# Kernel tuning notes

Hardware: AMD Instinct MI355X
Metric: run time of the kernel (lower is better)

Reference implementation:

```python
import jax, jax.numpy as jnp
import numpy as np

D_MODEL, N_HEADS, LATENT, ROPE = 4096, 128, 512, 64
HEAD_DIM = D_MODEL // N_HEADS  # 32
B, S = 2, 1024


def setup_inputs() -> dict:
    key = jax.random.key(0)
    ks = jax.random.split(key, 9)
    def w(k, i, o):
        return jax.random.normal(k, (i, o), dtype=jnp.float32) * (1.0 / np.sqrt(i))
    return {
        "x": jax.random.normal(ks[0], (B, S, D_MODEL), dtype=jnp.float32),
        "Wq_down": w(ks[1], D_MODEL, LATENT),
        "Wq_up": w(ks[2], LATENT, N_HEADS * HEAD_DIM),
        "Wq_rope": w(ks[3], D_MODEL, N_HEADS * ROPE),
        "Wkv_down": w(ks[4], D_MODEL, LATENT),
        "Wk_up": w(ks[5], LATENT, N_HEADS * HEAD_DIM),
        "Wv_up": w(ks[6], LATENT, N_HEADS * HEAD_DIM),
        "Wk_rope": w(ks[7], D_MODEL, ROPE),
        "Wo": w(ks[8], N_HEADS * HEAD_DIM, D_MODEL),
    }


def reference(x, Wq_down, Wq_up, Wq_rope, Wkv_down, Wk_up, Wv_up, Wk_rope, Wo):
    b, s, _ = x.shape
    # latent down-projections
    c_q = x @ Wq_down                                   # [B,S,latent]
    c_kv = x @ Wkv_down                                 # [B,S,latent]
    # up-projections, reshaped to per-head
    q_c = (c_q @ Wq_up).reshape(b, s, N_HEADS, HEAD_DIM)    # [B,S,H,Dh]
    q_r = (x @ Wq_rope).reshape(b, s, N_HEADS, ROPE)        # [B,S,H,Dr]
    k_c = (c_kv @ Wk_up).reshape(b, s, N_HEADS, HEAD_DIM)   # [B,S,H,Dh]
    v_c = (c_kv @ Wv_up).reshape(b, s, N_HEADS, HEAD_DIM)   # [B,S,H,Dh]
    k_r = x @ Wk_rope                                       # [B,S,Dr] shared over heads
    scale = jnp.asarray((HEAD_DIM + ROPE) ** 0.5, x.dtype)
    # scores = q.k with q=[q_c|q_r], k=[k_c|k_r(broadcast)] -> split the dot product
    scores = (jnp.einsum("bqhd,bkhd->bhqk", q_c, k_c)
              + jnp.einsum("bqhd,bkd->bhqk", q_r, k_r)) / scale  # [B,H,S,S]
    attn = jax.nn.softmax(scores, axis=-1)
    out = jnp.einsum("bhqk,bkhd->bqhd", attn, v_c)          # [B,S,H,Dh]
    out = out.reshape(b, s, N_HEADS * HEAD_DIM)
    return out @ Wo                                         # [B,S,d_model]
```

## Files before the change

kernel.cpp:

```cpp
#include <hip/hip_runtime.h>
#include <hip/hip_bf16.h>
#include <math.h>

#define D_MODEL 4096
#define N_HEADS 128
#define LATENT  512
#define ROPE_D  64
#define HEAD_D  32
#define BATCH   2
#define SEQ     1024
#define NTOK    (BATCH*SEQ)

typedef unsigned short u16;
typedef __attribute__((ext_vector_type(8))) short bf16x8;
typedef __attribute__((ext_vector_type(4))) float f32x4;

__device__ __forceinline__ u16 f2bf(float f) {
    union { float f; unsigned u; } v; v.f = f;
    unsigned r = (v.u + 0x7fffu + ((v.u >> 16) & 1u)) >> 16;
    return (u16)r;
}

__device__ __forceinline__ void gl_lds16(const u16* g, u16* l) {
    __builtin_amdgcn_global_load_lds(
        (const __attribute__((address_space(1))) unsigned int*)g,
        (__attribute__((address_space(3))) unsigned int*)l, 16, 0, 0);
}

__device__ __forceinline__ void castT_tile(const float* __restrict__ W,
                                           u16* __restrict__ Wt,
                                           int K, int N, int jx, int jy,
                                           float (*tile)[33])
{
    const int tid = threadIdx.x;
    const int j0 = jx * 32, i0 = jy * 32;
    {
        int r = tid >> 3, c4 = (tid & 7) << 2;
        float4 v = *(const float4*)(W + (size_t)(i0 + r) * N + j0 + c4);
        tile[r][c4 + 0] = v.x; tile[r][c4 + 1] = v.y;
        tile[r][c4 + 2] = v.z; tile[r][c4 + 3] = v.w;
    }
    __syncthreads();
    {
        int n = tid >> 3, k4 = (tid & 7) << 2;
        u16 o[4] = { f2bf(tile[k4 + 0][n]), f2bf(tile[k4 + 1][n]),
                     f2bf(tile[k4 + 2][n]), f2bf(tile[k4 + 3][n]) };
        *(uint2*)(Wt + (size_t)(j0 + n) * K + i0 + k4) = *(uint2*)o;
    }
}

template<int MODE>
__device__ __forceinline__ void gemm_core(const u16* __restrict__ A,
                                          const u16* __restrict__ Bt,
                                          void* __restrict__ Cout,
                                          int N, int K, int lda, int ldb, int ldc,
                                          int bm, int bn, u16* As, u16* Bs)
{
    const int tid  = threadIdx.x;
    const int lane = tid & 63;
    const int wave = tid >> 6;
    const int wr = wave >> 1, wc = wave & 1;
    const int l15 = lane & 15, lg = lane >> 4;

    f32x4 acc[4][4];
    #pragma unroll
    for (int i = 0; i < 4; ++i)
        #pragma unroll
        for (int j = 0; j < 4; ++j) acc[i][j] = (f32x4){0.f, 0.f, 0.f, 0.f};

    for (int kt = 0; kt < K; kt += 64) {
        __syncthreads();
        #pragma unroll
        for (int i = 0; i < 4; ++i) {
            int f = i * 256 + tid;
            int row = f >> 3, c = f & 7;
            int sc = c ^ (row & 7);
            gl_lds16(A + (size_t)(bm + row) * lda + kt + sc * 8, As + f * 8);
        }
        #pragma unroll
        for (int i = 0; i < 4; ++i) {
            int f = i * 256 + tid;
            int row = f >> 3, c = f & 7;
            int sc = c ^ (row & 7);
            gl_lds16(Bt + (size_t)(bn + row) * ldb + kt + sc * 8, Bs + f * 8);
        }
        __syncthreads();

        #pragma unroll
        for (int t = 0; t < 2; ++t) {
            bf16x8 af[4], bf[4];
            #pragma unroll
            for (int fm = 0; fm < 4; ++fm) {
                int row = wr * 64 + fm * 16 + l15;
                int c = (t * 4 + lg) ^ (row & 7);
                af[fm] = *(const bf16x8*)(As + row * 64 + c * 8);
            }
            #pragma unroll
            for (int fn = 0; fn < 4; ++fn) {
                int row = wc * 64 + fn * 16 + l15;
                int c = (t * 4 + lg) ^ (row & 7);
                bf[fn] = *(const bf16x8*)(Bs + row * 64 + c * 8);
            }
            #pragma unroll
            for (int fm = 0; fm < 4; ++fm)
                #pragma unroll
                for (int fn = 0; fn < 4; ++fn)
                    acc[fm][fn] = __builtin_amdgcn_mfma_f32_16x16x32_bf16(
                        af[fm], bf[fn], acc[fm][fn], 0, 0, 0);
        }
    }

    #pragma unroll
    for (int fm = 0; fm < 4; ++fm)
        #pragma unroll
        for (int fn = 0; fn < 4; ++fn)
            #pragma unroll
            for (int ri = 0; ri < 4; ++ri) {
                int row = bm + wr * 64 + fm * 16 + 4 * lg + ri;
                int col = bn + wc * 64 + fn * 16 + l15;
                if (col < N) {
                    float v = acc[fm][fn][ri];
                    if (MODE == 1) ((float*)Cout)[(size_t)row * ldc + col] = v;
                    else           ((u16*)Cout)[(size_t)row * ldc + col] = f2bf(v);
                }
            }
}

template<int MODE>
__global__ __launch_bounds__(256)
void gemm_bf16(const u16* __restrict__ A, const u16* __restrict__ Bt,
               void* __restrict__ Cout, int N, int K,
               int lda, int ldb, int ldc)
{
    __shared__ __align__(16) u16 As[128 * 64];
    __shared__ __align__(16) u16 Bs[128 * 64];
    const int nwg  = gridDim.x * gridDim.y;
    const int orig = blockIdx.y * gridDim.x + blockIdx.x;
    const int swz  = (orig & 7) * (nwg >> 3) + (orig >> 3);
    const int bm = (swz % gridDim.y) * 128;
    const int bn = (swz / gridDim.y) * 128;
    gemm_core<MODE>(A, Bt, Cout, N, K, lda, ldb, ldc, bm, bn, As, Bs);
}

__global__ __launch_bounds__(256)
void prep_kernel(const float* __restrict__ x, u16* __restrict__ xb,
                 const float* __restrict__ Wq_rope, const float* __restrict__ Wq_down,
                 const float* __restrict__ Wkv_down, const float* __restrict__ Wk_rope,
                 const float* __restrict__ Wk_up, const float* __restrict__ Wv_up,
                 const float* __restrict__ Wq_up,
                 u16* __restrict__ BigT, u16* __restrict__ UpT, u16* __restrict__ WuqT)
{
    __shared__ float tile[32][33];
    const int tid = threadIdx.x;
    int id = blockIdx.x;
    if (id < 4096) {
        size_t i = ((size_t)id * 256 + tid) * 8;
        float4 a = *(const float4*)(x + i);
        float4 b = *(const float4*)(x + i + 4);
        u16 o[8] = {f2bf(a.x), f2bf(a.y), f2bf(a.z), f2bf(a.w),
                    f2bf(b.x), f2bf(b.y), f2bf(b.z), f2bf(b.w)};
        *(bf16x8*)(xb + i) = *(bf16x8*)o;
        return;
    }
    id -= 4096;
    if (id < 32768) { castT_tile(Wq_rope, BigT, 4096, 8192, id & 255, id >> 8, tile); return; }
    id -= 32768;
    if (id < 2048) { castT_tile(Wq_down, BigT + (size_t)8192 * 4096, 4096, 512, id & 15, id >> 4, tile); return; }
    id -= 2048;
    if (id < 2048) { castT_tile(Wkv_down, BigT + (size_t)8704 * 4096, 4096, 512, id & 15, id >> 4, tile); return; }
    id -= 2048;
    if (id < 256) { castT_tile(Wk_rope, BigT + (size_t)9216 * 4096, 4096, 64, id & 1, id >> 1, tile); return; }
    id -= 256;
    if (id < 2048) { castT_tile(Wk_up, UpT, 512, 4096, id & 127, id >> 7, tile); return; }
    id -= 2048;
    if (id < 2048) { castT_tile(Wv_up, UpT + (size_t)4096 * 512, 512, 4096, id & 127, id >> 7, tile); return; }
    id -= 2048;
    if (id < 2048) { castT_tile(Wq_up, WuqT, 512, 4096, id & 127, id >> 7, tile); return; }
    id -= 2048;
    {
        u16* dst = BigT + ((size_t)9280 + id) * 4096;
        bf16x8 z = (bf16x8){0, 0, 0, 0, 0, 0, 0, 0};
        *(bf16x8*)(dst + tid * 8) = z;
        *(bf16x8*)(dst + 2048 + tid * 8) = z;
    }
}

__global__ __launch_bounds__(256)
void fused2_kernel(const u16* __restrict__ Cbig, const u16* __restrict__ UpT,
                   u16* __restrict__ C2, const u16* __restrict__ WuqT,
                   u16* __restrict__ q_c, const float* __restrict__ Wo,
                   u16* __restrict__ WoT)
{
    __shared__ __align__(16) u16 As[128 * 64];
    __shared__ __align__(16) u16 Bs[128 * 64];
    int id = blockIdx.x;
    if (id < 1024) {
        const int swz = (id & 7) * 128 + (id >> 3);
        const int bm = (swz & 15) * 128, bn = (swz >> 4) * 128;
        gemm_core<0>(Cbig + 8704, UpT, C2, 8192, 512, 9344, 512, 8192, bm, bn, As, Bs);
        return;
    }
    id -= 1024;
    if (id < 512) {
        const int swz = (id & 7) * 64 + (id >> 3);
        const int bm = (swz & 15) * 128, bn = (swz >> 4) * 128;
        gemm_core<0>(Cbig + 8192, WuqT, q_c, 4096, 512, 9344, 512, 4096, bm, bn, As, Bs);
        return;
    }
    id -= 512;
    {
        float (*tile)[33] = reinterpret_cast<float(*)[33]>(As);
        castT_tile(Wo, WoT, 4096, 4096, id & 127, id >> 7, tile);
    }
}

__global__ __launch_bounds__(256)
void vtrans_kernel(const u16* __restrict__ vc, u16* __restrict__ vt)
{
    __shared__ __align__(16) u16 tile[64][72];
    const int tid = threadIdx.x;
    const int c0 = blockIdx.x * 64;
    const int s0 = blockIdx.y * 64;
    const int b  = blockIdx.z;
    #pragma unroll
    for (int it = 0; it < 2; ++it) {
        int e = it * 256 + tid;
        int r = e >> 3, c8 = e & 7;
        *(bf16x8*)&tile[r][c8 * 8] =
            *(const bf16x8*)(vc + (size_t)(b * SEQ + s0 + r) * 8192 + c0 + c8 * 8);
    }
    __syncthreads();
    #pragma unroll
    for (int it = 0; it < 2; ++it) {
        int e = it * 256 + tid;
        int d = e >> 3, c8 = e & 7;
        u16 o[8];
        #pragma unroll
        for (int j = 0; j < 8; ++j) o[j] = tile[c8 * 8 + j][d];
        *(bf16x8*)(vt + (size_t)(b * D_MODEL + c0 + d) * SEQ + s0 + c8 * 8) = *(bf16x8*)o;
    }
}

__global__ __launch_bounds__(256)
void attn_kernel(const u16* __restrict__ q_c, const u16* __restrict__ q_r,
                 const u16* __restrict__ k_c, const u16* __restrict__ k_r,
                 const u16* __restrict__ vt,  u16* __restrict__ attn_out)
{
    __shared__ __align__(16) u16 s_kc[2][64 * 32];
    __shared__ __align__(16) u16 s_kr[2][64 * 64];
    __shared__ __align__(16) u16 s_vt[2][32 * 64];
    __shared__ __align__(16) u16 s_p[4][16 * 64];
    __shared__ __align__(16) u16 s_one[16 * 64];

    const int tid  = threadIdx.x;
    const int lane = tid & 63;
    const int w    = tid >> 6;
    const int l15  = lane & 15, lg = lane >> 4;
    const int q0 = blockIdx.x * 64;
    const int h  = blockIdx.y;
    const int b  = blockIdx.z;
    const size_t bS = (size_t)b * SEQ;
    const int hc = h * HEAD_D;
    const float c2 = 0.1020620726159658f * 1.44269504088896f;

    const int qrow = q0 + w * 16 + l15;
    const bf16x8 qf0 = *(const bf16x8*)(q_c + (bS + qrow) * 4096 + hc + lg * 8);
    const bf16x8 qf1 = *(const bf16x8*)(q_r + (bS + qrow) * 9344 + h * ROPE_D + lg * 8);
    const bf16x8 qf2 = *(const bf16x8*)(q_r + (bS + qrow) * 9344 + h * ROPE_D + 32 + lg * 8);

    float m2 = -1e30f;
    f32x4 oacc[3];
    oacc[0] = (f32x4){0.f, 0.f, 0.f, 0.f};
    oacc[1] = (f32x4){0.f, 0.f, 0.f, 0.f};
    oacc[2] = (f32x4){0.f, 0.f, 0.f, 0.f};

    auto stage = [&](int buf, int k0) {
        { int f = tid, r = f >> 2, c = f & 3;
          gl_lds16(k_c + (bS + k0 + r) * 8192 + hc + ((c ^ ((r >> 1) & 3)) << 3),
                   &s_kc[buf][f * 8]); }
        #pragma unroll
        for (int it = 0; it < 2; ++it) {
          int f = it * 256 + tid, r = f >> 3, c = f & 7;
          gl_lds16(k_r + (bS + k0 + r) * 9344 + ((c ^ (r & 7)) << 3),
                   &s_kr[buf][f * 8]); }
        { int f = tid, d = f >> 3, c = f & 7;
          gl_lds16(vt + ((size_t)b * D_MODEL + hc + d) * SEQ + k0 + ((c ^ (d & 7)) << 3),
                   &s_vt[buf][f * 8]); }
    };

    {
        unsigned v = (tid < 16) ? 0x3F803F80u : 0u;
        *(uint2*)&s_one[tid * 4] = make_uint2(v, v);
    }
    stage(0, 0);
    asm volatile("s_waitcnt vmcnt(0) lgkmcnt(0)" ::: "memory");
    __builtin_amdgcn_sched_barrier(0);
    __builtin_amdgcn_s_barrier();
    __builtin_amdgcn_sched_barrier(0);

    int cur = 0;
    for (int t = 0; t < SEQ / 64; ++t) {
        if (t + 1 < SEQ / 64) {
            stage(cur ^ 1, (t + 1) * 64);
            asm volatile("s_waitcnt vmcnt(4)" ::: "memory");
        } else {
            asm volatile("s_waitcnt vmcnt(0)" ::: "memory");
        }
        __builtin_amdgcn_sched_barrier(0);
        __builtin_amdgcn_s_barrier();
        __builtin_amdgcn_sched_barrier(0);

        f32x4 sc[4];
        #pragma unroll
        for (int fc = 0; fc < 4; ++fc) sc[fc] = (f32x4){0.f, 0.f, 0.f, 0.f};
        __builtin_amdgcn_s_setprio(1);
        #pragma unroll
        for (int fc = 0; fc < 4; ++fc) {
            int row = fc * 16 + l15;
            bf16x8 kb = *(const bf16x8*)&s_kc[cur][row * 32 + ((lg ^ ((row >> 1) & 3)) << 3)];
            sc[fc] = __builtin_amdgcn_mfma_f32_16x16x32_bf16(kb, qf0, sc[fc], 0, 0, 0);
        }
        #pragma unroll
        for (int tt = 0; tt < 2; ++tt) {
            bf16x8 qf = tt ? qf2 : qf1;
            #pragma unroll
            for (int fc = 0; fc < 4; ++fc) {
                int row = fc * 16 + l15;
                bf16x8 kb = *(const bf16x8*)&s_kr[cur][row * 64 + (((tt * 4 + lg) ^ (row & 7)) << 3)];
                sc[fc] = __builtin_amdgcn_mfma_f32_16x16x32_bf16(kb, qf, sc[fc], 0, 0, 0);
            }
        }
        __builtin_amdgcn_s_setprio(0);

        float a0 = fmaxf(fmaxf(sc[0][0], sc[0][1]), sc[0][2]);
        float a1 = fmaxf(fmaxf(sc[0][3], sc[1][0]), sc[1][1]);
        float a2 = fmaxf(fmaxf(sc[1][2], sc[1][3]), sc[2][0]);
        float a3 = fmaxf(fmaxf(sc[2][1], sc[2][2]), sc[2][3]);
        float a4 = fmaxf(fmaxf(sc[3][0], sc[3][1]), sc[3][2]);
        float b0 = fmaxf(fmaxf(a0, a1), a2);
        float b1 = fmaxf(fmaxf(a3, a4), sc[3][3]);
        float tmx = fmaxf(b0, b1);
        tmx = fmaxf(tmx, __shfl_xor(tmx, 16));
        tmx = fmaxf(tmx, __shfl_xor(tmx, 32));
        float tl2 = tmx * c2;
        if (!__all(tl2 <= m2 + 8.f)) {
            float mn = fmaxf(m2, tl2);
            float corr = exp2f(m2 - mn);
            m2 = mn;
            #pragma unroll
            for (int ri = 0; ri < 4; ++ri) {
                float cr = __shfl(corr, 4 * lg + ri);
                oacc[0][ri] *= cr; oacc[1][ri] *= cr; oacc[2][ri] *= cr;
            }
        }
        unsigned pk0[4], pk1[4];
        #pragma unroll
        for (int fc = 0; fc < 4; ++fc) {
            float p0 = exp2f(fmaf(sc[fc][0], c2, -m2));
            float p1 = exp2f(fmaf(sc[fc][1], c2, -m2));
            float p2 = exp2f(fmaf(sc[fc][2], c2, -m2));
            float p3 = exp2f(fmaf(sc[fc][3], c2, -m2));
            asm("v_cvt_pk_bf16_f32 %0, %1, %2" : "=v"(pk0[fc]) : "v"(p0), "v"(p1));
            asm("v_cvt_pk_bf16_f32 %0, %1, %2" : "=v"(pk1[fc]) : "v"(p2), "v"(p3));
        }
        #pragma unroll
        for (int fc = 0; fc < 4; ++fc) {
            int ch = (2 * fc + (lg >> 1)) ^ (l15 & 7);
            *(uint2*)&s_p[w][l15 * 64 + ch * 8 + 4 * (lg & 1)] =
                make_uint2(pk0[fc], pk1[fc]);
        }

        __builtin_amdgcn_s_setprio(1);
        #pragma unroll
        for (int t2 = 0; t2 < 2; ++t2) {
            bf16x8 pa = *(const bf16x8*)&s_p[w][l15 * 64 + (((t2 * 4 + lg) ^ (l15 & 7)) << 3)];
            #pragma unroll
            for (int fd = 0; fd < 2; ++fd) {
                int row = fd * 16 + l15;
                bf16x8 vb = *(const bf16x8*)&s_vt[cur][row * 64 + (((t2 * 4 + lg) ^ (row & 7)) << 3)];
                oacc[fd] = __builtin_amdgcn_mfma_f32_16x16x32_bf16(pa, vb, oacc[fd], 0, 0, 0);
            }
            bf16x8 vb1 = *(const bf16x8*)&s_one[l15 * 64 + (((t2 * 4 + lg) ^ (l15 & 7)) << 3)];
            oacc[2] = __builtin_amdgcn_mfma_f32_16x16x32_bf16(pa, vb1, oacc[2], 0, 0, 0);
        }
        __builtin_amdgcn_s_setprio(0);

        asm volatile("s_waitcnt lgkmcnt(0)" ::: "memory");
        __builtin_amdgcn_sched_barrier(0);
        __builtin_amdgcn_s_barrier();
        __builtin_amdgcn_sched_barrier(0);
        cur ^= 1;
    }

    #pragma unroll
    for (int ri = 0; ri < 4; ++ri) {
        float ls = __shfl(oacc[2][ri], lg << 4);
        float inv = 1.f / ls;
        int row = q0 + w * 16 + 4 * lg + ri;
        attn_out[(bS + row) * 4096 + hc + l15]      = f2bf(oacc[0][ri] * inv);
        attn_out[(bS + row) * 4096 + hc + 16 + l15] = f2bf(oacc[1][ri] * inv);
    }
}

extern "C" void kernel_launch(void* const* d_in, const int* in_sizes, int n_in,
                              void* d_out, int out_size, void* d_ws, size_t ws_size,
                              hipStream_t stream)
{
    (void)in_sizes; (void)n_in; (void)out_size; (void)ws_size;

    const float* x        = (const float*)d_in[0];
    const float* Wq_down  = (const float*)d_in[1];
    const float* Wq_up    = (const float*)d_in[2];
    const float* Wq_rope  = (const float*)d_in[3];
    const float* Wkv_down = (const float*)d_in[4];
    const float* Wk_up    = (const float*)d_in[5];
    const float* Wv_up    = (const float*)d_in[6];
    const float* Wk_rope  = (const float*)d_in[7];
    const float* Wo       = (const float*)d_in[8];

    u16* ws   = (u16*)d_ws;
    u16* xb   = ws;
    u16* BigT = xb + (size_t)8388608;
    u16* UpT  = BigT + (size_t)38797312;
    u16* WuqT = UpT + (size_t)4194304;
    u16* C_big= WuqT + (size_t)2097152;
    u16* C2   = C_big + (size_t)19136512;
    u16* WoT  = BigT;
    u16* vt   = BigT + (size_t)16777216;
    u16* q_c  = BigT + (size_t)25165824;
    u16* attn_out = xb;

    dim3 blk(256);

    hipLaunchKernelGGL(prep_kernel, dim3(47424), blk, 0, stream,
                       x, xb, Wq_rope, Wq_down, Wkv_down, Wk_rope,
                       Wk_up, Wv_up, Wq_up, BigT, UpT, WuqT);
    gemm_bf16<0><<<dim3(73, 16), blk, 0, stream>>>(
        xb, BigT, C_big, 9344, 4096, 4096, 4096, 9344);
    hipLaunchKernelGGL(fused2_kernel, dim3(1024 + 512 + 16384), blk, 0, stream,
                       C_big, UpT, C2, WuqT, q_c, Wo, WoT);
    hipLaunchKernelGGL(vtrans_kernel, dim3(64, 16, 2), blk, 0, stream, C2 + 4096, vt);
    hipLaunchKernelGGL(attn_kernel, dim3(16, 128, 2), blk, 0, stream,
                       q_c, C_big, C2, C_big + 9216, vt, attn_out);
    gemm_bf16<1><<<dim3(32, 16), blk, 0, stream>>>(
        attn_out, WoT, d_out, 4096, 4096, 4096, 4096, 4096);
}
```

Before: 522.3 us.

## Process two query tiles per attention block and fuse up-weight casts into first GEMM

The attention kernel now handles 128 query rows per block, two 16-row sub-tiles per wave, so each staged K/V tile in LDS feeds twice as many MFMAs. This halves global K/V traffic and the barrier count per query. The row-sum ones operand moves from LDS into a register constant. The online-softmax max now does the cross-lane shuffles only when a rescale is needed. Separately, the Wk_up/Wv_up/Wq_up transpose-casts move out of the prep kernel and run as extra blocks of the first GEMM launch, to fill the GEMM's tail. The cost is higher register pressure in attention, which may lower occupancy, and only 2048 attention blocks.

```diff
diff --git a/kernel.cpp b/kernel.cpp
--- a/kernel.cpp
+++ b/kernel.cpp
@@ -143,12 +143,36 @@
 }
 
 __global__ __launch_bounds__(256)
+void gemm1_fused(const u16* __restrict__ xb, const u16* __restrict__ BigT,
+                 u16* __restrict__ C_big,
+                 const float* __restrict__ Wk_up, const float* __restrict__ Wv_up,
+                 const float* __restrict__ Wq_up,
+                 u16* __restrict__ UpT, u16* __restrict__ WuqT)
+{
+    __shared__ __align__(16) u16 As[128 * 64];
+    __shared__ __align__(16) u16 Bs[128 * 64];
+    int id = blockIdx.x;
+    if (id < 1168) {
+        const int swz = (id & 7) * 146 + (id >> 3);
+        const int bm = (swz % 16) * 128;
+        const int bn = (swz / 16) * 128;
+        gemm_core<0>(xb, BigT, C_big, 9344, 4096, 4096, 4096, 9344, bm, bn, As, Bs);
+        return;
+    }
+    id -= 1168;
+    float (*tile)[33] = reinterpret_cast<float(*)[33]>(As);
+    if (id < 2048) { castT_tile(Wk_up, UpT, 512, 4096, id & 127, id >> 7, tile); return; }
+    id -= 2048;
+    if (id < 2048) { castT_tile(Wv_up, UpT + (size_t)4096 * 512, 512, 4096, id & 127, id >> 7, tile); return; }
+    id -= 2048;
+    castT_tile(Wq_up, WuqT, 512, 4096, id & 127, id >> 7, tile);
+}
+
+__global__ __launch_bounds__(256)
 void prep_kernel(const float* __restrict__ x, u16* __restrict__ xb,
                  const float* __restrict__ Wq_rope, const float* __restrict__ Wq_down,
                  const float* __restrict__ Wkv_down, const float* __restrict__ Wk_rope,
-                 const float* __restrict__ Wk_up, const float* __restrict__ Wv_up,
-                 const float* __restrict__ Wq_up,
-                 u16* __restrict__ BigT, u16* __restrict__ UpT, u16* __restrict__ WuqT)
+                 u16* __restrict__ BigT)
 {
     __shared__ float tile[32][33];
     const int tid = threadIdx.x;
@@ -171,12 +195,6 @@
     id -= 2048;
     if (id < 256) { castT_tile(Wk_rope, BigT + (size_t)9216 * 4096, 4096, 64, id & 1, id >> 1, tile); return; }
     id -= 256;
-    if (id < 2048) { castT_tile(Wk_up, UpT, 512, 4096, id & 127, id >> 7, tile); return; }
-    id -= 2048;
-    if (id < 2048) { castT_tile(Wv_up, UpT + (size_t)4096 * 512, 512, 4096, id & 127, id >> 7, tile); return; }
-    id -= 2048;
-    if (id < 2048) { castT_tile(Wq_up, WuqT, 512, 4096, id & 127, id >> 7, tile); return; }
-    id -= 2048;
     {
         u16* dst = BigT + ((size_t)9280 + id) * 4096;
         bf16x8 z = (bf16x8){0, 0, 0, 0, 0, 0, 0, 0};
@@ -249,30 +267,41 @@
     __shared__ __align__(16) u16 s_kc[2][64 * 32];
     __shared__ __align__(16) u16 s_kr[2][64 * 64];
     __shared__ __align__(16) u16 s_vt[2][32 * 64];
-    __shared__ __align__(16) u16 s_p[4][16 * 64];
-    __shared__ __align__(16) u16 s_one[16 * 64];
+    __shared__ __align__(16) u16 s_p[4][2][16 * 64];
 
     const int tid  = threadIdx.x;
     const int lane = tid & 63;
     const int w    = tid >> 6;
     const int l15  = lane & 15, lg = lane >> 4;
-    const int q0 = blockIdx.x * 64;
+    const int q0 = blockIdx.x * 128;
     const int h  = blockIdx.y;
     const int b  = blockIdx.z;
     const size_t bS = (size_t)b * SEQ;
     const int hc = h * HEAD_D;
     const float c2 = 0.1020620726159658f * 1.44269504088896f;
 
-    const int qrow = q0 + w * 16 + l15;
-    const bf16x8 qf0 = *(const bf16x8*)(q_c + (bS + qrow) * 4096 + hc + lg * 8);
-    const bf16x8 qf1 = *(const bf16x8*)(q_r + (bS + qrow) * 9344 + h * ROPE_D + lg * 8);
-    const bf16x8 qf2 = *(const bf16x8*)(q_r + (bS + qrow) * 9344 + h * ROPE_D + 32 + lg * 8);
-
-    float m2 = -1e30f;
-    f32x4 oacc[3];
-    oacc[0] = (f32x4){0.f, 0.f, 0.f, 0.f};
-    oacc[1] = (f32x4){0.f, 0.f, 0.f, 0.f};
-    oacc[2] = (f32x4){0.f, 0.f, 0.f, 0.f};
+    const int qA = q0 + w * 16 + l15;
+    const int qB = qA + 64;
+    const bf16x8 qfA0 = *(const bf16x8*)(q_c + (bS + qA) * 4096 + hc + lg * 8);
+    const bf16x8 qfA1 = *(const bf16x8*)(q_r + (bS + qA) * 9344 + h * ROPE_D + lg * 8);
+    const bf16x8 qfA2 = *(const bf16x8*)(q_r + (bS + qA) * 9344 + h * ROPE_D + 32 + lg * 8);
+    const bf16x8 qfB0 = *(const bf16x8*)(q_c + (bS + qB) * 4096 + hc + lg * 8);
+    const bf16x8 qfB1 = *(const bf16x8*)(q_r + (bS + qB) * 9344 + h * ROPE_D + lg * 8);
+    const bf16x8 qfB2 = *(const bf16x8*)(q_r + (bS + qB) * 9344 + h * ROPE_D + 32 + lg * 8);
+
+    bf16x8 vone;
+    {
+        short o = (l15 == 0) ? (short)0x3F80 : (short)0;
+        vone = (bf16x8){o, o, o, o, o, o, o, o};
+    }
+
+    float m2A = -1e30f, m2B = -1e30f;
+    f32x4 oaccA[3], oaccB[3];
+    #pragma unroll
+    for (int i = 0; i < 3; ++i) {
+        oaccA[i] = (f32x4){0.f, 0.f, 0.f, 0.f};
+        oaccB[i] = (f32x4){0.f, 0.f, 0.f, 0.f};
+    }
 
     auto stage = [&](int buf, int k0) {
         { int f = tid, r = f >> 2, c = f & 3;
@@ -288,12 +317,8 @@
                    &s_vt[buf][f * 8]); }
     };
 
-    {
-        unsigned v = (tid < 16) ? 0x3F803F80u : 0u;
-        *(uint2*)&s_one[tid * 4] = make_uint2(v, v);
-    }
     stage(0, 0);
-    asm volatile("s_waitcnt vmcnt(0) lgkmcnt(0)" ::: "memory");
+    asm volatile("s_waitcnt vmcnt(0)" ::: "memory");
     __builtin_amdgcn_sched_barrier(0);
     __builtin_amdgcn_s_barrier();
     __builtin_amdgcn_sched_barrier(0);
@@ -310,78 +335,93 @@
         __builtin_amdgcn_s_barrier();
         __builtin_amdgcn_sched_barrier(0);
 
-        f32x4 sc[4];
-        #pragma unroll
-        for (int fc = 0; fc < 4; ++fc) sc[fc] = (f32x4){0.f, 0.f, 0.f, 0.f};
+        f32x4 scA[4], scB[4];
+        #pragma unroll
+        for (int fc = 0; fc < 4; ++fc) {
+            scA[fc] = (f32x4){0.f, 0.f, 0.f, 0.f};
+            scB[fc] = (f32x4){0.f, 0.f, 0.f, 0.f};
+        }
         __builtin_amdgcn_s_setprio(1);
         #pragma unroll
         for (int fc = 0; fc < 4; ++fc) {
             int row = fc * 16 + l15;
             bf16x8 kb = *(const bf16x8*)&s_kc[cur][row * 32 + ((lg ^ ((row >> 1) & 3)) << 3)];
-            sc[fc] = __builtin_amdgcn_mfma_f32_16x16x32_bf16(kb, qf0, sc[fc], 0, 0, 0);
+            scA[fc] = __builtin_amdgcn_mfma_f32_16x16x32_bf16(kb, qfA0, scA[fc], 0, 0, 0);
+            scB[fc] = __builtin_amdgcn_mfma_f32_16x16x32_bf16(kb, qfB0, scB[fc], 0, 0, 0);
         }
         #pragma unroll
         for (int tt = 0; tt < 2; ++tt) {
-            bf16x8 qf = tt ? qf2 : qf1;
+            bf16x8 qa = tt ? qfA2 : qfA1;
+            bf16x8 qb = tt ? qfB2 : qfB1;
             #pragma unroll
             for (int fc = 0; fc < 4; ++fc) {
                 int row = fc * 16 + l15;
                 bf16x8 kb = *(const bf16x8*)&s_kr[cur][row * 64 + (((tt * 4 + lg) ^ (row & 7)) << 3)];
-                sc[fc] = __builtin_amdgcn_mfma_f32_16x16x32_bf16(kb, qf, sc[fc], 0, 0, 0);
+                scA[fc] = __builtin_amdgcn_mfma_f32_16x16x32_bf16(kb, qa, scA[fc], 0, 0, 0);
+                scB[fc] = __builtin_amdgcn_mfma_f32_16x16x32_bf16(kb, qb, scB[fc], 0, 0, 0);
             }
         }
         __builtin_amdgcn_s_setprio(0);
 
-        float a0 = fmaxf(fmaxf(sc[0][0], sc[0][1]), sc[0][2]);
-        float a1 = fmaxf(fmaxf(sc[0][3], sc[1][0]), sc[1][1]);
-        float a2 = fmaxf(fmaxf(sc[1][2], sc[1][3]), sc[2][0]);
-        float a3 = fmaxf(fmaxf(sc[2][1], sc[2][2]), sc[2][3]);
-        float a4 = fmaxf(fmaxf(sc[3][0], sc[3][1]), sc[3][2]);
-        float b0 = fmaxf(fmaxf(a0, a1), a2);
-        float b1 = fmaxf(fmaxf(a3, a4), sc[3][3]);
-        float tmx = fmaxf(b0, b1);
-        tmx = fmaxf(tmx, __shfl_xor(tmx, 16));
-        tmx = fmaxf(tmx, __shfl_xor(tmx, 32));
-        float tl2 = tmx * c2;
-        if (!__all(tl2 <= m2 + 8.f)) {
-            float mn = fmaxf(m2, tl2);
-            float corr = exp2f(m2 - mn);
-            m2 = mn;
-            #pragma unroll
-            for (int ri = 0; ri < 4; ++ri) {
-                float cr = __shfl(corr, 4 * lg + ri);
-                oacc[0][ri] *= cr; oacc[1][ri] *= cr; oacc[2][ri] *= cr;
-            }
-        }
-        unsigned pk0[4], pk1[4];
-        #pragma unroll
-        for (int fc = 0; fc < 4; ++fc) {
-            float p0 = exp2f(fmaf(sc[fc][0], c2, -m2));
-            float p1 = exp2f(fmaf(sc[fc][1], c2, -m2));
-            float p2 = exp2f(fmaf(sc[fc][2], c2, -m2));
-            float p3 = exp2f(fmaf(sc[fc][3], c2, -m2));
-            asm("v_cvt_pk_bf16_f32 %0, %1, %2" : "=v"(pk0[fc]) : "v"(p0), "v"(p1));
-            asm("v_cvt_pk_bf16_f32 %0, %1, %2" : "=v"(pk1[fc]) : "v"(p2), "v"(p3));
-        }
-        #pragma unroll
-        for (int fc = 0; fc < 4; ++fc) {
-            int ch = (2 * fc + (lg >> 1)) ^ (l15 & 7);
-            *(uint2*)&s_p[w][l15 * 64 + ch * 8 + 4 * (lg & 1)] =
-                make_uint2(pk0[fc], pk1[fc]);
+        #pragma unroll
+        for (int st = 0; st < 2; ++st) {
+            f32x4* sc = st ? scB : scA;
+            float& m2 = st ? m2B : m2A;
+            f32x4* oacc = st ? oaccB : oaccA;
+
+            float a0 = fmaxf(fmaxf(sc[0][0], sc[0][1]), sc[0][2]);
+            float a1 = fmaxf(fmaxf(sc[0][3], sc[1][0]), sc[1][1]);
+            float a2 = fmaxf(fmaxf(sc[1][2], sc[1][3]), sc[2][0]);
+            float a3 = fmaxf(fmaxf(sc[2][1], sc[2][2]), sc[2][3]);
+            float a4 = fmaxf(fmaxf(sc[3][0], sc[3][1]), sc[3][2]);
+            float b0 = fmaxf(fmaxf(a0, a1), a2);
+            float b1 = fmaxf(fmaxf(a3, a4), sc[3][3]);
+            float lmx = fmaxf(b0, b1);
+            if (!__all(lmx * c2 <= m2 + 8.f)) {
+                float tmx = fmaxf(lmx, __shfl_xor(lmx, 16));
+                tmx = fmaxf(tmx, __shfl_xor(tmx, 32));
+                float mn = fmaxf(m2, tmx * c2);
+                float corr = exp2f(m2 - mn);
+                m2 = mn;
+                #pragma unroll
+                for (int ri = 0; ri < 4; ++ri) {
+                    float cr = __shfl(corr, 4 * lg + ri);
+                    oacc[0][ri] *= cr; oacc[1][ri] *= cr; oacc[2][ri] *= cr;
+                }
+            }
+            unsigned pk0[4], pk1[4];
+            #pragma unroll
+            for (int fc = 0; fc < 4; ++fc) {
+                float p0 = exp2f(fmaf(sc[fc][0], c2, -m2));
+                float p1 = exp2f(fmaf(sc[fc][1], c2, -m2));
+                float p2 = exp2f(fmaf(sc[fc][2], c2, -m2));
+                float p3 = exp2f(fmaf(sc[fc][3], c2, -m2));
+                asm("v_cvt_pk_bf16_f32 %0, %1, %2" : "=v"(pk0[fc]) : "v"(p0), "v"(p1));
+                asm("v_cvt_pk_bf16_f32 %0, %1, %2" : "=v"(pk1[fc]) : "v"(p2), "v"(p3));
+            }
+            #pragma unroll
+            for (int fc = 0; fc < 4; ++fc) {
+                int ch = (2 * fc + (lg >> 1)) ^ (l15 & 7);
+                *(uint2*)&s_p[w][st][l15 * 64 + ch * 8 + 4 * (lg & 1)] =
+                    make_uint2(pk0[fc], pk1[fc]);
+            }
         }
 
         __builtin_amdgcn_s_setprio(1);
         #pragma unroll
         for (int t2 = 0; t2 < 2; ++t2) {
-            bf16x8 pa = *(const bf16x8*)&s_p[w][l15 * 64 + (((t2 * 4 + lg) ^ (l15 & 7)) << 3)];
+            int pofs = (((t2 * 4 + lg) ^ (l15 & 7)) << 3);
+            bf16x8 paA = *(const bf16x8*)&s_p[w][0][l15 * 64 + pofs];
+            bf16x8 paB = *(const bf16x8*)&s_p[w][1][l15 * 64 + pofs];
             #pragma unroll
             for (int fd = 0; fd < 2; ++fd) {
                 int row = fd * 16 + l15;
                 bf16x8 vb = *(const bf16x8*)&s_vt[cur][row * 64 + (((t2 * 4 + lg) ^ (row & 7)) << 3)];
-                oacc[fd] = __builtin_amdgcn_mfma_f32_16x16x32_bf16(pa, vb, oacc[fd], 0, 0, 0);
-            }
-            bf16x8 vb1 = *(const bf16x8*)&s_one[l15 * 64 + (((t2 * 4 + lg) ^ (l15 & 7)) << 3)];
-            oacc[2] = __builtin_amdgcn_mfma_f32_16x16x32_bf16(pa, vb1, oacc[2], 0, 0, 0);
+                oaccA[fd] = __builtin_amdgcn_mfma_f32_16x16x32_bf16(paA, vb, oaccA[fd], 0, 0, 0);
+                oaccB[fd] = __builtin_amdgcn_mfma_f32_16x16x32_bf16(paB, vb, oaccB[fd], 0, 0, 0);
+            }
+            oaccA[2] = __builtin_amdgcn_mfma_f32_16x16x32_bf16(paA, vone, oaccA[2], 0, 0, 0);
+            oaccB[2] = __builtin_amdgcn_mfma_f32_16x16x32_bf16(paB, vone, oaccB[2], 0, 0, 0);
         }
         __builtin_amdgcn_s_setprio(0);
 
@@ -394,11 +434,15 @@
 
     #pragma unroll
     for (int ri = 0; ri < 4; ++ri) {
-        float ls = __shfl(oacc[2][ri], lg << 4);
-        float inv = 1.f / ls;
-        int row = q0 + w * 16 + 4 * lg + ri;
-        attn_out[(bS + row) * 4096 + hc + l15]      = f2bf(oacc[0][ri] * inv);
-        attn_out[(bS + row) * 4096 + hc + 16 + l15] = f2bf(oacc[1][ri] * inv);
+        float lsA = __shfl(oaccA[2][ri], lg << 4);
+        float lsB = __shfl(oaccB[2][ri], lg << 4);
+        float invA = 1.f / lsA, invB = 1.f / lsB;
+        int rowA = q0 + w * 16 + 4 * lg + ri;
+        int rowB = rowA + 64;
+        attn_out[(bS + rowA) * 4096 + hc + l15]      = f2bf(oaccA[0][ri] * invA);
+        attn_out[(bS + rowA) * 4096 + hc + 16 + l15] = f2bf(oaccA[1][ri] * invA);
+        attn_out[(bS + rowB) * 4096 + hc + l15]      = f2bf(oaccB[0][ri] * invB);
+        attn_out[(bS + rowB) * 4096 + hc + 16 + l15] = f2bf(oaccB[1][ri] * invB);
     }
 }
 
@@ -432,15 +476,14 @@
 
     dim3 blk(256);
 
-    hipLaunchKernelGGL(prep_kernel, dim3(47424), blk, 0, stream,
-                       x, xb, Wq_rope, Wq_down, Wkv_down, Wk_rope,
-                       Wk_up, Wv_up, Wq_up, BigT, UpT, WuqT);
-    gemm_bf16<0><<<dim3(73, 16), blk, 0, stream>>>(
-        xb, BigT, C_big, 9344, 4096, 4096, 4096, 9344);
+    hipLaunchKernelGGL(prep_kernel, dim3(41280), blk, 0, stream,
+                       x, xb, Wq_rope, Wq_down, Wkv_down, Wk_rope, BigT);
+    hipLaunchKernelGGL(gemm1_fused, dim3(1168 + 6144), blk, 0, stream,
+                       xb, BigT, C_big, Wk_up, Wv_up, Wq_up, UpT, WuqT);
     hipLaunchKernelGGL(fused2_kernel, dim3(1024 + 512 + 16384), blk, 0, stream,
                        C_big, UpT, C2, WuqT, q_c, Wo, WoT);
     hipLaunchKernelGGL(vtrans_kernel, dim3(64, 16, 2), blk, 0, stream, C2 + 4096, vt);
-    hipLaunchKernelGGL(attn_kernel, dim3(16, 128, 2), blk, 0, stream,
+    hipLaunchKernelGGL(attn_kernel, dim3(8, 128, 2), blk, 0, stream,
                        q_c, C_big, C2, C_big + 9216, vt, attn_out);
     gemm_bf16<1><<<dim3(32, 16), blk, 0, stream>>>(
         attn_out, WoT, d_out, 4096, 4096, 4096, 4096, 4096);
```

New measurement: 508.6 us, median of 2. 1.03x faster.
